# Optimization experiments

Hardware: AMD Instinct MI355X
Metric: run time of the kernel (lower is better)

Reference implementation:

```python
import jax, jax.numpy as jnp
import numpy as np

B, S, M, D, H, NH = 8, 1024, 2048, 512, 512, 8  # batch, seq, mem slots, memory_dim, hidden_dim, heads
THRESHOLD = 0.5
DECAY = 0.95


def setup_inputs() -> dict:
    key = jax.random.key(0)
    ks = jax.random.split(key, 16)
    def w(k, shape, s=0.02):
        return jax.random.normal(k, shape, jnp.float32) * s
    z = lambda n: jnp.zeros((n,), jnp.float32)
    return {
        'new_info': jax.random.normal(ks[0], (B, S, D), jnp.float32),
        'memory_bank': jax.random.normal(ks[1], (B, M, D), jnp.float32),
        'W_in': w(ks[2], (D, H)), 'b_in': z(H),
        'Wq': w(ks[3], (H, H)), 'bq': z(H),
        'Wk': w(ks[4], (H, H)), 'bk': z(H),
        'Wv': w(ks[5], (H, H)), 'bv': z(H),
        'Wo': w(ks[6], (H, H)), 'bo': z(H),
        'Wi1': w(ks[7], (H, H // 2)), 'bi1': z(H // 2),
        'Wi2': w(ks[8], (H // 2, 1)), 'bi2': z(1),
        'Wu1': w(ks[9], (2 * H, H)), 'bu1': z(H),
        'Wu2': w(ks[10], (H, H)), 'bu2': z(H),
    }


def _mha(q, k, v, Wq, bq, Wk, bk, Wv, bv, Wo, bo):
    # torch nn.MultiheadAttention math (batch_first, eval mode / no dropout)
    b, mq, h = q.shape
    d = h // NH
    qh = (q @ Wq + bq).reshape(b, mq, NH, d)
    kh = (k @ Wk + bk).reshape(b, -1, NH, d)
    vh = (v @ Wv + bv).reshape(b, -1, NH, d)
    scores = jnp.einsum('bqhd,bkhd->bhqk', qh, kh) / np.float32(np.sqrt(d))
    attn = jax.nn.softmax(scores, axis=-1)
    out = jnp.einsum('bhqk,bkhd->bqhd', attn, vh).reshape(b, mq, h)
    return out @ Wo + bo


def reference(new_info, memory_bank, W_in, b_in, Wq, bq, Wk, bk, Wv, bv, Wo, bo,
              Wi1, bi1, Wi2, bi2, Wu1, bu1, Wu2, bu2):
    # project new info + memory into hidden space
    info_proj = new_info @ W_in + b_in                       # [B,S,H]
    mem_proj = memory_bank @ W_in + b_in                     # [B,M,H]
    # per-token importance (sigmoid MLP)
    imp = jax.nn.sigmoid(jax.nn.relu(info_proj @ Wi1 + bi1) @ Wi2 + bi2)[..., 0]  # [B,S]
    # cross-attention: memory slots attend to new tokens -> per-slot write weights
    attn_out = _mha(mem_proj, info_proj, info_proj, Wq, bq, Wk, bk, Wv, bv, Wo, bo)  # [B,M,H]
    # scale write weights by importance (vectorized reading of the original broadcast)
    write_weights = attn_out * jnp.mean(imp, axis=1)[:, None, None]  # [B,M,H]
    # write-position selection: argmax over memory slots (importance scalar is positive,
    # so in the original all qualifying tokens of a batch pick the same slot)
    pos = jnp.argmax(jnp.mean(write_weights, axis=-1), axis=1)      # [B]
    mask = imp > THRESHOLD                                          # [B,S]
    exists = jnp.any(mask, axis=1)                                  # [B]
    # original loop overwrites the slot for each qualifying s, always reading the
    # ORIGINAL memory_bank -> final value comes from the LAST qualifying token
    s_star = S - 1 - jnp.argmax(mask[:, ::-1], axis=1)              # [B]
    bidx = jnp.arange(B)
    sel = new_info[bidx, s_star]                                    # [B,D]
    old = memory_bank[bidx, pos]                                    # [B,D]
    comb = jnp.concatenate([old, sel], axis=-1)                     # [B,2D]
    upd = jnp.tanh(jax.nn.relu(comb @ Wu1 + bu1) @ Wu2 + bu2)       # [B,H]
    ww = write_weights[bidx, pos]                                   # [B,H]
    new_mem = jnp.where(exists[:, None], old + upd * ww, old)
    updated = memory_bank.at[bidx, pos].set(new_mem)
    # forgetting: memory_age defaults to zeros -> decay_rate**0 == 1 (kept for fidelity)
    decay = jnp.power(jnp.float32(DECAY), jnp.zeros((M,), jnp.float32))
    updated = updated * decay[None, :, None]
    return updated, write_weights, imp
```

## Files before the change

### kernel.cpp

```cpp
#include <hip/hip_runtime.h>
#include <hip/hip_bf16.h>
#include <math.h>

#define BB 8
#define SS 1024
#define MM 2048
#define DD 512
#define HH 512
#define NHEAD 8
#define DHEAD 64

typedef __attribute__((ext_vector_type(8))) short short8;
typedef __attribute__((ext_vector_type(4))) float f32x4;
typedef unsigned short us;

__device__ __forceinline__ us bf_hi(float x) {
    __hip_bfloat16 h = __float2bfloat16(x);
    return *reinterpret_cast<const us*>(&h);
}
__device__ __forceinline__ float bf_f(us h) {
    return __uint_as_float(((unsigned)h) << 16);
}
__device__ __forceinline__ void split_pack4(float a, float b, float c, float d,
                                            uint2& hp, uint2& lp) {
    us h0 = bf_hi(a), h1 = bf_hi(b), h2 = bf_hi(c), h3 = bf_hi(d);
    hp.x = (unsigned)h0 | ((unsigned)h1 << 16);
    hp.y = (unsigned)h2 | ((unsigned)h3 << 16);
    us l0 = bf_hi(a - bf_f(h0)), l1 = bf_hi(b - bf_f(h1));
    us l2 = bf_hi(c - bf_f(h2)), l3 = bf_hi(d - bf_f(h3));
    lp.x = (unsigned)l0 | ((unsigned)l1 << 16);
    lp.y = (unsigned)l2 | ((unsigned)l3 << 16);
}
__device__ __forceinline__ uint2 pack4_hi(float a, float b, float c, float d) {
    uint2 hp;
    hp.x = (unsigned)bf_hi(a) | ((unsigned)bf_hi(b) << 16);
    hp.y = (unsigned)bf_hi(c) | ((unsigned)bf_hi(d) << 16);
    return hp;
}

__device__ __forceinline__ void gload_lds16(const void* g, void* l) {
    __builtin_amdgcn_global_load_lds(
        (__attribute__((address_space(1))) void*)(g),
        (__attribute__((address_space(3))) void*)(l), 16, 0, 0);
}

struct TSB {
    const float* src[6];
    us* dh[6];
    us* dl[6];
    int nc[6];
};

__global__ __launch_bounds__(256) void prep_all(
    const float* __restrict__ x, float* __restrict__ cpy,
    us* __restrict__ hi, us* __restrict__ lo, int n8, float* __restrict__ zbuf,
    const float* __restrict__ bk, const float* __restrict__ bv,
    float* __restrict__ bkv,
    const float* __restrict__ b_in, const float* __restrict__ Wq,
    const float* __restrict__ bq, float* __restrict__ bq_eff, TSB a)
{
    __shared__ float tile[32][33];
    const int blk = blockIdx.x, tid = threadIdx.x;
    if (blk >= 2066) {
        const int t = blk - 2066;
        const int wsel = t >> 8;
        const int n0 = (t & 15) * 32, k0 = ((t >> 4) & 15) * 32;
        const int ncols = a.nc[wsel];
        if (n0 >= ncols) return;
        const float* W = a.src[wsel];
        {
            const int r = tid >> 3, c = (tid & 7) * 4;
            const float4 v = *(const float4*)(W + (size_t)(k0 + r) * ncols + n0 + c);
            tile[r][c + 0] = v.x; tile[r][c + 1] = v.y;
            tile[r][c + 2] = v.z; tile[r][c + 3] = v.w;
        }
        __syncthreads();
        {
            const int n = tid >> 3, k = (tid & 7) * 4;
            uint2 hp, lp;
            split_pack4(tile[k + 0][n], tile[k + 1][n], tile[k + 2][n], tile[k + 3][n], hp, lp);
            *(uint2*)(a.dh[wsel] + (size_t)(n0 + n) * 512 + k0 + k) = hp;
            *(uint2*)(a.dl[wsel] + (size_t)(n0 + n) * 512 + k0 + k) = lp;
        }
        return;
    }
    if (blk >= 2064) {
        const int n = (blk - 2064) * 256 + tid;
        float v = bq[n];
        for (int k = 0; k < 512; ++k) v = fmaf(b_in[k], Wq[(size_t)k * 512 + n], v);
        bq_eff[n] = v;
        return;
    }
    if (blk >= 2060) {
        const int i = (blk - 2060) * 256 + tid;
        bkv[i] = (i < 512) ? bk[i] : bv[i - 512];
        return;
    }
    if (blk >= 2048) {
        const int i = (blk - 2048) * 2048 + tid * 8;
        *(float4*)(zbuf + i) = make_float4(0.f, 0.f, 0.f, 0.f);
        *(float4*)(zbuf + i + 4) = make_float4(0.f, 0.f, 0.f, 0.f);
        return;
    }
    const int stride = 2048 * 256;
    for (int i = blk * 256 + tid; i < n8; i += stride) {
        const float4 va = *(const float4*)(x + (size_t)i * 8);
        const float4 vb = *(const float4*)(x + (size_t)i * 8 + 4);
        *(float4*)(cpy + (size_t)i * 8) = va;
        *(float4*)(cpy + (size_t)i * 8 + 4) = vb;
        uint2 h0, l0, h1, l1;
        split_pack4(va.x, va.y, va.z, va.w, h0, l0);
        split_pack4(vb.x, vb.y, vb.z, vb.w, h1, l1);
        *(uint2*)(hi + (size_t)i * 8) = h0;
        *(uint2*)(hi + (size_t)i * 8 + 4) = h1;
        *(uint2*)(lo + (size_t)i * 8) = l0;
        *(uint2*)(lo + (size_t)i * 8 + 4) = l1;
    }
}

#define GEMM_F32A_BODY(K_)                                                          \
    f32x4 acc[4][4];                                                                \
    _Pragma("unroll")                                                               \
    for (int i = 0; i < 4; ++i)                                                     \
        _Pragma("unroll")                                                           \
        for (int j = 0; j < 4; ++j)                                                 \
            _Pragma("unroll")                                                       \
            for (int r = 0; r < 4; ++r) acc[i][j][r] = 0.f;                         \
    const int ar = tid >> 4;                                                        \
    const int ak = (tid & 15) * 4;                                                  \
    int bsrow[4], bsf[4], bsoff[4];                                                 \
    _Pragma("unroll")                                                               \
    for (int it = 0; it < 4; ++it) {                                                \
        const int s = tid + 256 * it;                                               \
        bsrow[it] = s >> 3;                                                         \
        bsf[it] = s & 7;                                                            \
        bsoff[it] = bsrow[it] * 64 + ((bsf[it] ^ (bsrow[it] & 7)) << 3);            \
    }                                                                               \
    for (int k0 = 0; k0 < (K_); k0 += 64) {                                         \
        __syncthreads();                                                            \
        _Pragma("unroll")                                                           \
        for (int p = 0; p < 8; ++p) {                                               \
            const int r = p * 16 + ar;                                              \
            const float4 av = *(const float4*)(A + (size_t)(m0 + r) * (K_) + k0 + ak); \
            const int aoff = r * 128 + (((ak >> 3) ^ (r & 7)) << 4) + ((tid & 1) << 3); \
            uint2 hp, lp;                                                           \
            split_pack4(av.x, av.y, av.z, av.w, hp, lp);                            \
            *(uint2*)((char*)sAh + aoff) = hp;                                      \
            *(uint2*)((char*)sAl + aoff) = lp;                                      \
        }                                                                           \
        _Pragma("unroll")                                                           \
        for (int it = 0; it < 4; ++it) {                                            \
            const size_t bo = (size_t)(n0 + bsrow[it]) * (K_) + k0 + bsf[it] * 8;   \
            *(uint4*)(sBh + bsoff[it]) = *(const uint4*)(Bh + bo);                  \
            *(uint4*)(sBl + bsoff[it]) = *(const uint4*)(Bl + bo);                  \
        }                                                                           \
        __syncthreads();                                                            \
        _Pragma("unroll")                                                           \
        for (int ks = 0; ks < 2; ++ks) {                                            \
            short8 afh[4], afl[4], bfh[4], bfl[4];                                  \
            _Pragma("unroll")                                                       \
            for (int i = 0; i < 4; ++i) {                                           \
                const int row = wm * 64 + i * 16 + fr;                              \
                const int off = row * 128 + (((ks * 4 + fq4) ^ (row & 7)) << 4);    \
                afh[i] = *(const short8*)((const char*)sAh + off);                  \
                afl[i] = *(const short8*)((const char*)sAl + off);                  \
            }                                                                       \
            _Pragma("unroll")                                                       \
            for (int j = 0; j < 4; ++j) {                                           \
                const int row = wn * 64 + j * 16 + fr;                              \
                const int off = row * 128 + (((ks * 4 + fq4) ^ (row & 7)) << 4);    \
                bfh[j] = *(const short8*)((const char*)sBh + off);                  \
                bfl[j] = *(const short8*)((const char*)sBl + off);                  \
            }                                                                       \
            _Pragma("unroll")                                                       \
            for (int i = 0; i < 4; ++i)                                             \
                _Pragma("unroll")                                                   \
                for (int j = 0; j < 4; ++j) {                                       \
                    acc[i][j] = __builtin_amdgcn_mfma_f32_16x16x32_bf16(afh[i], bfh[j], acc[i][j], 0, 0, 0); \
                    acc[i][j] = __builtin_amdgcn_mfma_f32_16x16x32_bf16(afh[i], bfl[j], acc[i][j], 0, 0, 0); \
                    acc[i][j] = __builtin_amdgcn_mfma_f32_16x16x32_bf16(afl[i], bfh[j], acc[i][j], 0, 0, 0); \
                }                                                                   \
        }                                                                           \
    }

__global__ __launch_bounds__(256) void gemm_info_winq(
    const float* __restrict__ new_info,
    const us* __restrict__ wtin_h, const us* __restrict__ wtin_l,
    const float* __restrict__ b_in,
    us* __restrict__ Oh, us* __restrict__ Ol,
    const float* __restrict__ W_in,
    const us* __restrict__ wtq_h, const us* __restrict__ wtq_l,
    us* __restrict__ wtinq_h, us* __restrict__ wtinq_l)
{
    __shared__ us sm[32768];
    us* sAh = sm;            us* sAl = sm + 8192;
    us* sBh = sm + 16384;    us* sBl = sm + 24576;
    const int tid = threadIdx.x, lane = tid & 63;
    const int wid = tid >> 6, wm = wid >> 1, wn = wid & 1;
    const int fr = lane & 15, fq4 = lane >> 4;
    const int id = blockIdx.x;
    const bool isInfo = (id < 256);
    int m0, n0;
    const float* A;
    const us *Bh, *Bl;
    if (isInfo) {
        m0 = (id >> 2) * 128; n0 = (id & 3) * 128;
        A = new_info; Bh = wtin_h; Bl = wtin_l;
    } else {
        const int t = id - 256;
        m0 = (t >> 2) * 128; n0 = (t & 3) * 128;
        A = W_in; Bh = wtq_h; Bl = wtq_l;
    }
    GEMM_F32A_BODY(512)

    if (isInfo) {
#pragma unroll
        for (int j = 0; j < 4; ++j) {
            const int col = n0 + wn * 64 + j * 16 + fr;
            const float bj = b_in[col];
#pragma unroll
            for (int i = 0; i < 4; ++i)
#pragma unroll
                for (int r = 0; r < 4; ++r) {
                    const int row = m0 + wm * 64 + i * 16 + fq4 * 4 + r;
                    const float v = acc[i][j][r] + bj;
                    const us hv = bf_hi(v);
                    Oh[(size_t)row * 512 + col] = hv;
                    Ol[(size_t)row * 512 + col] = bf_hi(v - bf_f(hv));
                }
        }
    } else {
#pragma unroll
        for (int j = 0; j < 4; ++j) {
            const int col = n0 + wn * 64 + j * 16 + fr;
#pragma unroll
            for (int i = 0; i < 4; ++i)
#pragma unroll
                for (int r = 0; r < 4; ++r) {
                    const int row = m0 + wm * 64 + i * 16 + fq4 * 4 + r;
                    const float v = acc[i][j][r];
                    const us hv = bf_hi(v);
                    wtinq_h[(size_t)col * 512 + row] = hv;
                    wtinq_l[(size_t)col * 512 + row] = bf_hi(v - bf_f(hv));
                }
        }
    }
}

#define GEMM_PS_CORE(AhP, AlP, BhP, BlP, rsA_, K_)                                  \
    us* sAh = sm;            us* sAl = sm + 8192;                                   \
    us* sBh = sm + 16384;    us* sBl = sm + 24576;                                  \
    f32x4 acc[4][4];                                                                \
    _Pragma("unroll")                                                               \
    for (int i = 0; i < 4; ++i)                                                     \
        _Pragma("unroll")                                                           \
        for (int j = 0; j < 4; ++j)                                                 \
            _Pragma("unroll")                                                       \
            for (int r = 0; r < 4; ++r) acc[i][j][r] = 0.f;                         \
    const int fp = lane & 7, rsub = lane >> 3;                                      \
    const us* gsrc = (wid == 0) ? (AhP) : (wid == 1) ? (AlP)                        \
                   : (wid == 2) ? (BhP) : (BlP);                                    \
    const int grow0 = (wid < 2) ? m0 : n0;                                          \
    const int grs = (wid < 2) ? (rsA_) : (K_);                                      \
    us* lbase = sm + wid * 8192;                                                    \
    for (int k0 = 0; k0 < (K_); k0 += 64) {                                         \
        __syncthreads();                                                            \
        _Pragma("unroll")                                                           \
        for (int i = 0; i < 16; ++i) {                                              \
            const int row = i * 8 + rsub;                                           \
            const us* g = gsrc + (size_t)(grow0 + row) * grs + k0 +                 \
                          ((fp ^ (row & 7)) << 3);                                  \
            gload_lds16(g, lbase + i * 512);                                        \
        }                                                                           \
        __syncthreads();                                                            \
        _Pragma("unroll")                                                           \
        for (int ks = 0; ks < 2; ++ks) {                                            \
            short8 afh[4], afl[4], bfh[4], bfl[4];                                  \
            _Pragma("unroll")                                                       \
            for (int i = 0; i < 4; ++i) {                                           \
                const int row = wm * 64 + i * 16 + fr;                              \
                const int off = row * 128 + (((ks * 4 + fq4) ^ (row & 7)) << 4);    \
                afh[i] = *(const short8*)((const char*)sAh + off);                  \
                afl[i] = *(const short8*)((const char*)sAl + off);                  \
            }                                                                       \
            _Pragma("unroll")                                                       \
            for (int j = 0; j < 4; ++j) {                                           \
                const int row = wn * 64 + j * 16 + fr;                              \
                const int off = row * 128 + (((ks * 4 + fq4) ^ (row & 7)) << 4);    \
                bfh[j] = *(const short8*)((const char*)sBh + off);                  \
                bfl[j] = *(const short8*)((const char*)sBl + off);                  \
            }                                                                       \
            _Pragma("unroll")                                                       \
            for (int i = 0; i < 4; ++i)                                             \
                _Pragma("unroll")                                                   \
                for (int j = 0; j < 4; ++j) {                                       \
                    acc[i][j] = __builtin_amdgcn_mfma_f32_16x16x32_bf16(afh[i], bfh[j], acc[i][j], 0, 0, 0); \
                    acc[i][j] = __builtin_amdgcn_mfma_f32_16x16x32_bf16(afh[i], bfl[j], acc[i][j], 0, 0, 0); \
                    acc[i][j] = __builtin_amdgcn_mfma_f32_16x16x32_bf16(afl[i], bfh[j], acc[i][j], 0, 0, 0); \
                }                                                                   \
        }                                                                           \
    }

__global__ __launch_bounds__(256) void gemm_h1_logit(
    const us* __restrict__ Ah, const us* __restrict__ Al,
    const us* __restrict__ Bh, const us* __restrict__ Bl,
    const float* __restrict__ bias, const float* __restrict__ Wi2,
    float* __restrict__ logit)
{
    __shared__ us sm[32768];
    const int tid = threadIdx.x, lane = tid & 63;
    const int wid = tid >> 6, wm = wid >> 1, wn = wid & 1;
    const int fr = lane & 15, fq4 = lane >> 4;
    const int m0 = blockIdx.y * 128, n0 = blockIdx.x * 128;
    GEMM_PS_CORE(Ah, Al, Bh, Bl, 512, 512)

    float wsum[4][4];
#pragma unroll
    for (int i = 0; i < 4; ++i)
#pragma unroll
        for (int r = 0; r < 4; ++r) wsum[i][r] = 0.f;

#pragma unroll
    for (int j = 0; j < 4; ++j) {
        const int col = n0 + wn * 64 + j * 16 + fr;
        const float bj = bias[col];
        const float w2 = Wi2[col];
#pragma unroll
        for (int i = 0; i < 4; ++i)
#pragma unroll
            for (int r = 0; r < 4; ++r) {
                const float v = fmaxf(acc[i][j][r] + bj, 0.f);
                wsum[i][r] = fmaf(v, w2, wsum[i][r]);
            }
    }

    __syncthreads();
    float* red = (float*)sm;
    if (tid < 128) red[tid] = 0.f;
    __syncthreads();
#pragma unroll
    for (int i = 0; i < 4; ++i)
#pragma unroll
        for (int r = 0; r < 4; ++r)
            atomicAdd(&red[wm * 64 + i * 16 + fq4 * 4 + r], wsum[i][r]);
    __syncthreads();
    if (tid < 128) atomicAdd(&logit[m0 + tid], red[tid]);
}

__global__ __launch_bounds__(256) void impfin(
    const float* __restrict__ logit, const float* __restrict__ bi2,
    float* __restrict__ imp, float* __restrict__ imp_mean,
    int* __restrict__ s_star, int* __restrict__ exists)
{
    const int b = blockIdx.x, tid = threadIdx.x;
    const float b0 = bi2[0];
    float sum = 0.f; int last = -1;
    for (int s = tid; s < SS; s += 256) {
        const float ip = 1.0f / (1.0f + expf(-(logit[b * SS + s] + b0)));
        imp[b * SS + s] = ip;
        sum += ip;
        if (ip > 0.5f) last = s;
    }
#pragma unroll
    for (int m = 1; m < 64; m <<= 1) {
        sum += __shfl_xor(sum, m);
        last = max(last, __shfl_xor(last, m));
    }
    __shared__ float ssum[4]; __shared__ int slast[4];
    if ((tid & 63) == 0) { ssum[tid >> 6] = sum; slast[tid >> 6] = last; }
    __syncthreads();
    if (tid == 0) {
        const float t = ssum[0] + ssum[1] + ssum[2] + ssum[3];
        const int ml = max(max(slast[0], slast[1]), max(slast[2], slast[3]));
        imp_mean[b] = t / (float)SS;
        exists[b] = (ml >= 0) ? 1 : 0;
        s_star[b] = (ml >= 0) ? ml : (SS - 1);
    }
}

__global__ __launch_bounds__(256) void gemm_qkv_ps(
    const us* __restrict__ mbh, const us* __restrict__ mbl,
    const us* __restrict__ wtinq_h, const us* __restrict__ wtinq_l,
    const float* __restrict__ bq_eff,
    us* __restrict__ qsph, us* __restrict__ qspl,
    const us* __restrict__ iph, const us* __restrict__ ipl,
    const us* __restrict__ wtkv_h, const us* __restrict__ wtkv_l,
    const float* __restrict__ bkv,
    us* __restrict__ Kh, us* __restrict__ Kl,
    us* __restrict__ Vth, us* __restrict__ Vtl)
{
    __shared__ us sm[32768];
    const int tid = threadIdx.x, lane = tid & 63;
    const int wid = tid >> 6, wm = wid >> 1, wn = wid & 1;
    const int fr = lane & 15, fq4 = lane >> 4;
    const int id = blockIdx.x;
    const bool isQ = (id < 512);
    int m0, n0;
    const us *Ah, *Al, *Bh, *Bl;
    if (isQ) {
        m0 = (id >> 2) * 128; n0 = (id & 3) * 128;
        Ah = mbh; Al = mbl; Bh = wtinq_h; Bl = wtinq_l;
    } else {
        const int t = id - 512;
        m0 = (t >> 3) * 128; n0 = (t & 7) * 128;
        Ah = iph; Al = ipl; Bh = wtkv_h; Bl = wtkv_l;
    }
    GEMM_PS_CORE(Ah, Al, Bh, Bl, 512, 512)

    if (isQ) {
#pragma unroll
        for (int j = 0; j < 4; ++j) {
            const int col = n0 + wn * 64 + j * 16 + fr;
            const float bj = bq_eff[col];
#pragma unroll
            for (int i = 0; i < 4; ++i)
#pragma unroll
                for (int r = 0; r < 4; ++r) {
                    const int row = m0 + wm * 64 + i * 16 + fq4 * 4 + r;
                    const float v = acc[i][j][r] + bj;
                    const us hv = bf_hi(v);
                    qsph[(size_t)row * 512 + col] = hv;
                    qspl[(size_t)row * 512 + col] = bf_hi(v - bf_f(hv));
                }
        }
    } else if (n0 < 512) {
#pragma unroll
        for (int j = 0; j < 4; ++j) {
            const int col = n0 + wn * 64 + j * 16 + fr;
            const float bj = bkv[col];
#pragma unroll
            for (int i = 0; i < 4; ++i)
#pragma unroll
                for (int r = 0; r < 4; ++r) {
                    const int row = m0 + wm * 64 + i * 16 + fq4 * 4 + r;
                    const float v = (acc[i][j][r] + bj) * 0.125f;
                    const us hv = bf_hi(v);
                    Kh[(size_t)row * 512 + col] = hv;
                    Kl[(size_t)row * 512 + col] = bf_hi(v - bf_f(hv));
                }
        }
    } else {
#pragma unroll
        for (int j = 0; j < 4; ++j) {
            const int col = n0 + wn * 64 + j * 16 + fr;
            const float bj = bkv[col];
            const int d = col - 512;
#pragma unroll
            for (int i = 0; i < 4; ++i) {
                const int row0 = m0 + wm * 64 + i * 16 + fq4 * 4;
                uint2 hp, lp;
                split_pack4(acc[i][j][0] + bj, acc[i][j][1] + bj,
                            acc[i][j][2] + bj, acc[i][j][3] + bj, hp, lp);
                const size_t vo = ((size_t)(row0 >> 10) * 512 + d) * 1024 + (row0 & 1023);
                *(uint2*)(Vth + vo) = hp;
                *(uint2*)(Vtl + vo) = lp;
            }
        }
    }
}

__global__ __launch_bounds__(256) void gemm_wo_ps(
    const us* __restrict__ Ah, const us* __restrict__ Al,
    const us* __restrict__ Bh, const us* __restrict__ Bl,
    const float* __restrict__ bias, float* __restrict__ C,
    const float* __restrict__ rowscale, float* __restrict__ rowmeanv)
{
    __shared__ us sm[32768];
    const int tid = threadIdx.x, lane = tid & 63;
    const int wid = tid >> 6, wm = wid >> 1, wn = wid & 1;
    const int fr = lane & 15, fq4 = lane >> 4;
    const int m0 = blockIdx.y * 128, n0 = blockIdx.x * 128;
    GEMM_PS_CORE(Ah, Al, Bh, Bl, 512, 512)

    float rsum[4][4];
#pragma unroll
    for (int i = 0; i < 4; ++i)
#pragma unroll
        for (int r = 0; r < 4; ++r) rsum[i][r] = 0.f;

#pragma unroll
    for (int j = 0; j < 4; ++j) {
        const int col = n0 + wn * 64 + j * 16 + fr;
        const float bj = bias[col];
#pragma unroll
        for (int i = 0; i < 4; ++i)
#pragma unroll
            for (int r = 0; r < 4; ++r) {
                const int row = m0 + wm * 64 + i * 16 + fq4 * 4 + r;
                const float v = (acc[i][j][r] + bj) * rowscale[row / MM];
                C[(size_t)row * 512 + col] = v;
                rsum[i][r] += v;
            }
    }

    __syncthreads();
    float* red = (float*)sm;
    if (tid < 128) red[tid] = 0.f;
    __syncthreads();
#pragma unroll
    for (int i = 0; i < 4; ++i)
#pragma unroll
        for (int r = 0; r < 4; ++r)
            atomicAdd(&red[wm * 64 + i * 16 + fq4 * 4 + r], rsum[i][r]);
    __syncthreads();
    if (tid < 128) atomicAdd(&rowmeanv[m0 + tid], red[tid] * (1.0f / 512.0f));
}

__global__ __launch_bounds__(256) void attn_mfma(
    const us* __restrict__ Qh, const us* __restrict__ Ql,
    const us* __restrict__ Kh, const us* __restrict__ Kl,
    const us* __restrict__ Vth, const us* __restrict__ Vtl,
    us* __restrict__ aoh, us* __restrict__ aol)
{
    __shared__ us sm[20480];
    us* sKh = sm;            us* sKl = sm + 4096;
    us* sVh = sm + 8192;     us* sVl = sm + 12288;
    us* sPh = sm + 16384;

    const int tid = threadIdx.x, lane = tid & 63, w = tid >> 6;
    const int fr = lane & 15, fq4 = lane >> 4;

    const int wg = blockIdx.x;
    const int xcd = wg & 7, ix = wg >> 3;
    const int mt = ix & 31;
    const int pair = xcd + 8 * (ix >> 5);
    const int h = pair & 7, b = pair >> 3;
    const int m0 = mt * 64;

    const us* Qgh = Qh + ((size_t)(b * MM + m0)) * 512 + h * DHEAD;
    const us* Qgl = Ql + ((size_t)(b * MM + m0)) * 512 + h * DHEAD;
    const us* Kgh = Kh + ((size_t)b * SS) * 512 + h * DHEAD;
    const us* Kgl = Kl + ((size_t)b * SS) * 512 + h * DHEAD;
    const us* Vgh = Vth + ((size_t)b * 512 + h * DHEAD) * 1024;
    const us* Vgl = Vtl + ((size_t)b * 512 + h * DHEAD) * 1024;
    us* Oh = aoh + ((size_t)(b * MM + m0)) * 512 + h * DHEAD;
    us* Ol = aol + ((size_t)(b * MM + m0)) * 512 + h * DHEAD;

    short8 qfh[2], qfl[2];
#pragma unroll
    for (int ks = 0; ks < 2; ++ks) {
        const size_t qo = (size_t)(w * 16 + fr) * 512 + ks * 32 + fq4 * 8;
        qfh[ks] = *(const short8*)(Qgh + qo);
        qfl[ks] = *(const short8*)(Qgl + qo);
    }

    const int fp = lane & 7;
    const int rsub = lane >> 3;
    const bool isK = (w < 2);
    const us* gA = (w == 0) ? Kgh : (w == 1) ? Kgl : (w == 2) ? Vgh : Vgl;
    us* lbase = sm + w * 4096;

    f32x4 oacc[4];
#pragma unroll
    for (int j = 0; j < 4; ++j)
#pragma unroll
        for (int r = 0; r < 4; ++r) oacc[j][r] = 0.f;
    float mrun = -1e30f, lrun = 0.f;

    for (int t = 0; t < SS / 64; ++t) {
        __syncthreads();
        if (isK) {
#pragma unroll
            for (int i = 0; i < 8; ++i) {
                const int row = i * 8 + rsub;
                const us* g = gA + (size_t)(t * 64 + row) * 512 + ((fp ^ (row & 7)) << 3);
                gload_lds16(g, lbase + i * 512);
            }
        } else {
#pragma unroll
            for (int i = 0; i < 8; ++i) {
                const int row = i * 8 + rsub;
                const us* g = gA + (size_t)row * 1024 + t * 64 + ((fp ^ (row & 7)) << 3);
                gload_lds16(g, lbase + i * 512);
            }
        }
        __syncthreads();

        f32x4 stt[4];
#pragma unroll
        for (int fs = 0; fs < 4; ++fs)
#pragma unroll
            for (int r = 0; r < 4; ++r) stt[fs][r] = 0.f;
#pragma unroll
        for (int ks = 0; ks < 2; ++ks) {
            short8 kfh[4], kfl[4];
#pragma unroll
            for (int fs = 0; fs < 4; ++fs) {
                const int row = fs * 16 + fr;
                const int off = row * 128 + (((ks * 4 + fq4) ^ (row & 7)) << 4);
                kfh[fs] = *(const short8*)((const char*)sKh + off);
                kfl[fs] = *(const short8*)((const char*)sKl + off);
            }
#pragma unroll
            for (int fs = 0; fs < 4; ++fs) {
                stt[fs] = __builtin_amdgcn_mfma_f32_16x16x32_bf16(kfh[fs], qfh[ks], stt[fs], 0, 0, 0);
                stt[fs] = __builtin_amdgcn_mfma_f32_16x16x32_bf16(kfh[fs], qfl[ks], stt[fs], 0, 0, 0);
                stt[fs] = __builtin_amdgcn_mfma_f32_16x16x32_bf16(kfl[fs], qfh[ks], stt[fs], 0, 0, 0);
            }
        }

        float mx = stt[0][0];
#pragma unroll
        for (int fs = 0; fs < 4; ++fs)
#pragma unroll
            for (int r = 0; r < 4; ++r) mx = fmaxf(mx, stt[fs][r]);
        mx = fmaxf(mx, __shfl_xor(mx, 16));
        mx = fmaxf(mx, __shfl_xor(mx, 32));
        const bool grow = __any(mx > mrun);
        float scf = 1.f;
        if (grow) {
            const float nm = fmaxf(mrun, mx);
            scf = __expf(mrun - nm);
            mrun = nm;
        }
        float ps = 0.f;
#pragma unroll
        for (int fs = 0; fs < 4; ++fs)
#pragma unroll
            for (int r = 0; r < 4; ++r) {
                const float p = __expf(stt[fs][r] - mrun);
                stt[fs][r] = p;
                ps += p;
            }
        ps += __shfl_xor(ps, 16);
        ps += __shfl_xor(ps, 32);
        lrun = lrun * scf + ps;

#pragma unroll
        for (int fs = 0; fs < 4; ++fs) {
            const int q = w * 16 + fr;
            const int flog = (fs << 1) | (fq4 >> 1);
            const int off = q * 128 + ((flog ^ (q & 7)) << 4) + ((fq4 & 1) << 3);
            *(uint2*)((char*)sPh + off) = pack4_hi(stt[fs][0], stt[fs][1],
                                                  stt[fs][2], stt[fs][3]);
        }

        if (grow) {
#pragma unroll
            for (int r = 0; r < 4; ++r) {
                const float scv = __shfl(scf, fq4 * 4 + r);
#pragma unroll
                for (int fd = 0; fd < 4; ++fd) oacc[fd][r] *= scv;
            }
        }

#pragma unroll
        for (int ks = 0; ks < 2; ++ks) {
            short8 pfh, vfh[4], vfl[4];
            {
                const int row = w * 16 + fr;
                const int off = row * 128 + (((ks * 4 + fq4) ^ (row & 7)) << 4);
                pfh = *(const short8*)((const char*)sPh + off);
            }
#pragma unroll
            for (int fd = 0; fd < 4; ++fd) {
                const int row = fd * 16 + fr;
                const int off = row * 128 + (((ks * 4 + fq4) ^ (row & 7)) << 4);
                vfh[fd] = *(const short8*)((const char*)sVh + off);
                vfl[fd] = *(const short8*)((const char*)sVl + off);
            }
#pragma unroll
            for (int fd = 0; fd < 4; ++fd) {
                oacc[fd] = __builtin_amdgcn_mfma_f32_16x16x32_bf16(pfh, vfh[fd], oacc[fd], 0, 0, 0);
                oacc[fd] = __builtin_amdgcn_mfma_f32_16x16x32_bf16(pfh, vfl[fd], oacc[fd], 0, 0, 0);
            }
        }
    }

#pragma unroll
    for (int r = 0; r < 4; ++r) {
        const float inv = 1.0f / __shfl(lrun, fq4 * 4 + r);
        const int q = w * 16 + fq4 * 4 + r;
#pragma unroll
        for (int fd = 0; fd < 4; ++fd) {
            const float v = oacc[fd][r] * inv;
            const us hv = bf_hi(v);
            Oh[(size_t)q * 512 + fd * 16 + fr] = hv;
            Ol[(size_t)q * 512 + fd * 16 + fr] = bf_hi(v - bf_f(hv));
        }
    }
}

__global__ __launch_bounds__(256) void argmax_update(
    const float* __restrict__ rm,
    const float* __restrict__ mb, const float* __restrict__ ni,
    const float* __restrict__ Wu1, const float* __restrict__ bu1,
    const float* __restrict__ Wu2, const float* __restrict__ bu2,
    const float* __restrict__ wwp, const int* __restrict__ s_star,
    const int* __restrict__ exists, float* __restrict__ outu)
{
    const int b = blockIdx.x, tid = threadIdx.x;
    __shared__ float comb[2 * DD];
    __shared__ float hu[HH];
    __shared__ float sv[4]; __shared__ int si[4];
    __shared__ int spos;

    {
        float best = -3.0e38f; int bidx = 1 << 30;
        for (int m = tid; m < MM; m += 256) {
            const float v = rm[b * MM + m];
            if (v > best || (v == best && m < bidx)) { best = v; bidx = m; }
        }
#pragma unroll
        for (int msk = 1; msk < 64; msk <<= 1) {
            const float ov = __shfl_xor(best, msk);
            const int oi = __shfl_xor(bidx, msk);
            if (ov > best || (ov == best && oi < bidx)) { best = ov; bidx = oi; }
        }
        if ((tid & 63) == 0) { sv[tid >> 6] = best; si[tid >> 6] = bidx; }
        __syncthreads();
        if (tid == 0) {
            for (int w = 1; w < 4; ++w)
                if (sv[w] > best || (sv[w] == best && si[w] < bidx)) { best = sv[w]; bidx = si[w]; }
            spos = bidx;
        }
        __syncthreads();
    }

    const int p = spos, ss = s_star[b], ex = exists[b];
    const float* oldp = mb + ((size_t)(b * MM + p)) * DD;
    const float* selp = ni + ((size_t)(b * SS + ss)) * DD;
    for (int i = tid; i < DD; i += 256) { comb[i] = oldp[i]; comb[DD + i] = selp[i]; }
    __syncthreads();
#pragma unroll
    for (int t = 0; t < 2; ++t) {
        const int n = tid + t * 256;
        float a = bu1[n];
        for (int k = 0; k < 2 * DD; ++k) a = fmaf(comb[k], Wu1[(size_t)k * HH + n], a);
        hu[n] = fmaxf(a, 0.f);
    }
    __syncthreads();
#pragma unroll
    for (int t = 0; t < 2; ++t) {
        const int n = tid + t * 256;
        float a = bu2[n];
        for (int k = 0; k < HH; ++k) a = fmaf(hu[k], Wu2[(size_t)k * HH + n], a);
        const float upd = tanhf(a);
        const float wwv = wwp[((size_t)(b * MM + p)) * HH + n];
        const float ov = oldp[n];
        outu[((size_t)(b * MM + p)) * DD + n] = ex ? fmaf(upd, wwv, ov) : ov;
    }
}

extern "C" void kernel_launch(void* const* d_in, const int* in_sizes, int n_in,
                              void* d_out, int out_size, void* d_ws, size_t ws_size,
                              hipStream_t stream)
{
    const float* new_info    = (const float*)d_in[0];
    const float* memory_bank = (const float*)d_in[1];
    const float* W_in = (const float*)d_in[2];  const float* b_in = (const float*)d_in[3];
    const float* Wq   = (const float*)d_in[4];  const float* bq   = (const float*)d_in[5];
    const float* Wk   = (const float*)d_in[6];  const float* bk   = (const float*)d_in[7];
    const float* Wv   = (const float*)d_in[8];  const float* bv   = (const float*)d_in[9];
    const float* Wo   = (const float*)d_in[10]; const float* bo   = (const float*)d_in[11];
    const float* Wi1  = (const float*)d_in[12]; const float* bi1  = (const float*)d_in[13];
    const float* Wi2  = (const float*)d_in[14]; const float* bi2  = (const float*)d_in[15];
    const float* Wu1  = (const float*)d_in[16]; const float* bu1  = (const float*)d_in[17];
    const float* Wu2  = (const float*)d_in[18]; const float* bu2  = (const float*)d_in[19];

    float* out = (float*)d_out;
    float* out_updated = out;
    float* out_ww      = out + (size_t)BB * MM * HH;
    float* out_imp     = out + 2 * (size_t)BB * MM * HH;

    float* ws = (float*)d_ws;
    float* qsp_rg    = ws;
    float* ip_sp     = qsp_rg + 8388608;
    float* mb_sp     = ip_sp + 4194304;
    float* kvreg     = mb_sp + 8388608;
    float* wtf       = kvreg + 8388608;
    float* bq_eff    = wtf + 1703936;
    float* bkv       = bq_eff + 512;
    float* rowmeanv  = bkv + 1024;
    float* logit     = rowmeanv + 16384;
    float* imp_mean  = logit + 8192;
    int*   istar     = (int*)(imp_mean + BB);
    int*   iexists   = istar + BB;

    us* qsph = (us*)qsp_rg;
    us* qspl = qsph + 8388608;
    us* iph = (us*)ip_sp;
    us* ipl = iph + 4194304;
    us* mbh = (us*)mb_sp;
    us* mbl = mbh + 8388608;
    us* Kh  = (us*)kvreg;
    us* Kl  = Kh + 4194304;
    us* Vth = Kl + 4194304;
    us* Vtl = Vth + 4194304;

    us* wtin_h  = (us*)wtf;            us* wtin_l  = wtin_h + 262144;
    us* wtq_h   = wtin_l + 262144;     us* wtq_l   = wtq_h + 262144;
    us* wtkv_h  = wtq_l + 262144;      us* wtkv_l  = wtkv_h + 524288;
    us* wto_h   = wtkv_l + 524288;     us* wto_l   = wto_h + 262144;
    us* wtinq_h = wto_l + 262144;      us* wtinq_l = wtinq_h + 262144;
    us* wti1_h  = wtinq_l + 262144;    us* wti1_l  = wti1_h + 131072;

    const dim3 blk(256);

    TSB ts;
    ts.src[0] = W_in; ts.dh[0] = wtin_h;          ts.dl[0] = wtin_l;          ts.nc[0] = 512;
    ts.src[1] = Wq;   ts.dh[1] = wtq_h;           ts.dl[1] = wtq_l;           ts.nc[1] = 512;
    ts.src[2] = Wk;   ts.dh[2] = wtkv_h;          ts.dl[2] = wtkv_l;          ts.nc[2] = 512;
    ts.src[3] = Wv;   ts.dh[3] = wtkv_h + 262144; ts.dl[3] = wtkv_l + 262144; ts.nc[3] = 512;
    ts.src[4] = Wo;   ts.dh[4] = wto_h;           ts.dl[4] = wto_l;           ts.nc[4] = 512;
    ts.src[5] = Wi1;  ts.dh[5] = wti1_h;          ts.dl[5] = wti1_l;          ts.nc[5] = 256;
    prep_all<<<dim3(2066 + 1536), blk, 0, stream>>>(memory_bank, out_updated,
                                                    mbh, mbl, 1048576, rowmeanv,
                                                    bk, bv, bkv, b_in, Wq, bq,
                                                    bq_eff, ts);

    gemm_info_winq<<<dim3(272), blk, 0, stream>>>(new_info, wtin_h, wtin_l, b_in,
                                                  iph, ipl, W_in, wtq_h, wtq_l,
                                                  wtinq_h, wtinq_l);

    gemm_h1_logit<<<dim3(2, 64), blk, 0, stream>>>(iph, ipl, wti1_h, wti1_l,
                                                   bi1, Wi2, logit);

    impfin<<<dim3(BB), blk, 0, stream>>>(logit, bi2, out_imp,
                                         imp_mean, istar, iexists);

    gemm_qkv_ps<<<dim3(1024), blk, 0, stream>>>(mbh, mbl, wtinq_h, wtinq_l,
                                                bq_eff, qsph, qspl,
                                                iph, ipl, wtkv_h, wtkv_l, bkv,
                                                Kh, Kl, Vth, Vtl);

    attn_mfma<<<dim3(2048), blk, 0, stream>>>(qsph, qspl, Kh, Kl, Vth, Vtl,
                                              mbh, mbl);

    gemm_wo_ps<<<dim3(4, 128), blk, 0, stream>>>(mbh, mbl, wto_h, wto_l,
                                                 bo, out_ww, imp_mean, rowmeanv);

    argmax_update<<<dim3(BB), blk, 0, stream>>>(rowmeanv, memory_bank, new_info,
                                                Wu1, bu1, Wu2, bu2, out_ww,
                                                istar, iexists, out_updated);
}
```

Baseline: 424.1 us.

## Fold importance MLP GEMM and finalize into QKV and attention launches

Removes two kernel launches by appending the h1/logit GEMM tiles as extra blocks of the QKV projection kernel and the importance finalize as extra blocks of the attention kernel. Also raises wave priority around the attention MFMA loops and splits the update-MLP dot products into four independent accumulators to break the serial FMA dependency chain. This cuts launch gaps and small underfilled grids, at the cost of changing the summation order in the update MLP.

After: 409.1 us. -3.5%, faster.

```diff
diff --git a/kernel.cpp b/kernel.cpp
--- a/kernel.cpp
+++ b/kernel.cpp
@@ -301,84 +301,7 @@
         }                                                                           \
     }
 
-__global__ __launch_bounds__(256) void gemm_h1_logit(
-    const us* __restrict__ Ah, const us* __restrict__ Al,
-    const us* __restrict__ Bh, const us* __restrict__ Bl,
-    const float* __restrict__ bias, const float* __restrict__ Wi2,
-    float* __restrict__ logit)
-{
-    __shared__ us sm[32768];
-    const int tid = threadIdx.x, lane = tid & 63;
-    const int wid = tid >> 6, wm = wid >> 1, wn = wid & 1;
-    const int fr = lane & 15, fq4 = lane >> 4;
-    const int m0 = blockIdx.y * 128, n0 = blockIdx.x * 128;
-    GEMM_PS_CORE(Ah, Al, Bh, Bl, 512, 512)
-
-    float wsum[4][4];
-#pragma unroll
-    for (int i = 0; i < 4; ++i)
-#pragma unroll
-        for (int r = 0; r < 4; ++r) wsum[i][r] = 0.f;
-
-#pragma unroll
-    for (int j = 0; j < 4; ++j) {
-        const int col = n0 + wn * 64 + j * 16 + fr;
-        const float bj = bias[col];
-        const float w2 = Wi2[col];
-#pragma unroll
-        for (int i = 0; i < 4; ++i)
-#pragma unroll
-            for (int r = 0; r < 4; ++r) {
-                const float v = fmaxf(acc[i][j][r] + bj, 0.f);
-                wsum[i][r] = fmaf(v, w2, wsum[i][r]);
-            }
-    }
-
-    __syncthreads();
-    float* red = (float*)sm;
-    if (tid < 128) red[tid] = 0.f;
-    __syncthreads();
-#pragma unroll
-    for (int i = 0; i < 4; ++i)
-#pragma unroll
-        for (int r = 0; r < 4; ++r)
-            atomicAdd(&red[wm * 64 + i * 16 + fq4 * 4 + r], wsum[i][r]);
-    __syncthreads();
-    if (tid < 128) atomicAdd(&logit[m0 + tid], red[tid]);
-}
-
-__global__ __launch_bounds__(256) void impfin(
-    const float* __restrict__ logit, const float* __restrict__ bi2,
-    float* __restrict__ imp, float* __restrict__ imp_mean,
-    int* __restrict__ s_star, int* __restrict__ exists)
-{
-    const int b = blockIdx.x, tid = threadIdx.x;
-    const float b0 = bi2[0];
-    float sum = 0.f; int last = -1;
-    for (int s = tid; s < SS; s += 256) {
-        const float ip = 1.0f / (1.0f + expf(-(logit[b * SS + s] + b0)));
-        imp[b * SS + s] = ip;
-        sum += ip;
-        if (ip > 0.5f) last = s;
-    }
-#pragma unroll
-    for (int m = 1; m < 64; m <<= 1) {
-        sum += __shfl_xor(sum, m);
-        last = max(last, __shfl_xor(last, m));
-    }
-    __shared__ float ssum[4]; __shared__ int slast[4];
-    if ((tid & 63) == 0) { ssum[tid >> 6] = sum; slast[tid >> 6] = last; }
-    __syncthreads();
-    if (tid == 0) {
-        const float t = ssum[0] + ssum[1] + ssum[2] + ssum[3];
-        const int ml = max(max(slast[0], slast[1]), max(slast[2], slast[3]));
-        imp_mean[b] = t / (float)SS;
-        exists[b] = (ml >= 0) ? 1 : 0;
-        s_star[b] = (ml >= 0) ? ml : (SS - 1);
-    }
-}
-
-__global__ __launch_bounds__(256) void gemm_qkv_ps(
+__global__ __launch_bounds__(256) void gemm_qkvh1_ps(
     const us* __restrict__ mbh, const us* __restrict__ mbl,
     const us* __restrict__ wtinq_h, const us* __restrict__ wtinq_l,
     const float* __restrict__ bq_eff,
@@ -387,27 +310,33 @@
     const us* __restrict__ wtkv_h, const us* __restrict__ wtkv_l,
     const float* __restrict__ bkv,
     us* __restrict__ Kh, us* __restrict__ Kl,
-    us* __restrict__ Vth, us* __restrict__ Vtl)
+    us* __restrict__ Vth, us* __restrict__ Vtl,
+    const us* __restrict__ wti1_h, const us* __restrict__ wti1_l,
+    const float* __restrict__ bi1, const float* __restrict__ Wi2,
+    float* __restrict__ logit)
 {
     __shared__ us sm[32768];
     const int tid = threadIdx.x, lane = tid & 63;
     const int wid = tid >> 6, wm = wid >> 1, wn = wid & 1;
     const int fr = lane & 15, fq4 = lane >> 4;
     const int id = blockIdx.x;
-    const bool isQ = (id < 512);
     int m0, n0;
     const us *Ah, *Al, *Bh, *Bl;
-    if (isQ) {
+    if (id < 512) {
         m0 = (id >> 2) * 128; n0 = (id & 3) * 128;
         Ah = mbh; Al = mbl; Bh = wtinq_h; Bl = wtinq_l;
-    } else {
+    } else if (id < 1024) {
         const int t = id - 512;
         m0 = (t >> 3) * 128; n0 = (t & 7) * 128;
         Ah = iph; Al = ipl; Bh = wtkv_h; Bl = wtkv_l;
+    } else {
+        const int t = id - 1024;
+        m0 = (t >> 1) * 128; n0 = (t & 1) * 128;
+        Ah = iph; Al = ipl; Bh = wti1_h; Bl = wti1_l;
     }
     GEMM_PS_CORE(Ah, Al, Bh, Bl, 512, 512)
 
-    if (isQ) {
+    if (id < 512) {
 #pragma unroll
         for (int j = 0; j < 4; ++j) {
             const int col = n0 + wn * 64 + j * 16 + fr;
@@ -423,7 +352,7 @@
                     qspl[(size_t)row * 512 + col] = bf_hi(v - bf_f(hv));
                 }
         }
-    } else if (n0 < 512) {
+    } else if (id < 1024 && n0 < 512) {
 #pragma unroll
         for (int j = 0; j < 4; ++j) {
             const int col = n0 + wn * 64 + j * 16 + fr;
@@ -439,7 +368,7 @@
                     Kl[(size_t)row * 512 + col] = bf_hi(v - bf_f(hv));
                 }
         }
-    } else {
+    } else if (id < 1024) {
 #pragma unroll
         for (int j = 0; j < 4; ++j) {
             const int col = n0 + wn * 64 + j * 16 + fr;
@@ -456,6 +385,36 @@
                 *(uint2*)(Vtl + vo) = lp;
             }
         }
+    } else {
+        float wsum[4][4];
+#pragma unroll
+        for (int i = 0; i < 4; ++i)
+#pragma unroll
+            for (int r = 0; r < 4; ++r) wsum[i][r] = 0.f;
+#pragma unroll
+        for (int j = 0; j < 4; ++j) {
+            const int col = n0 + wn * 64 + j * 16 + fr;
+            const float bj = bi1[col];
+            const float w2 = Wi2[col];
+#pragma unroll
+            for (int i = 0; i < 4; ++i)
+#pragma unroll
+                for (int r = 0; r < 4; ++r) {
+                    const float v = fmaxf(acc[i][j][r] + bj, 0.f);
+                    wsum[i][r] = fmaf(v, w2, wsum[i][r]);
+                }
+        }
+        __syncthreads();
+        float* red = (float*)sm;
+        if (tid < 128) red[tid] = 0.f;
+        __syncthreads();
+#pragma unroll
+        for (int i = 0; i < 4; ++i)
+#pragma unroll
+            for (int r = 0; r < 4; ++r)
+                atomicAdd(&red[wm * 64 + i * 16 + fq4 * 4 + r], wsum[i][r]);
+        __syncthreads();
+        if (tid < 128) atomicAdd(&logit[m0 + tid], red[tid]);
     }
 }
 
@@ -510,14 +469,47 @@
     const us* __restrict__ Qh, const us* __restrict__ Ql,
     const us* __restrict__ Kh, const us* __restrict__ Kl,
     const us* __restrict__ Vth, const us* __restrict__ Vtl,
-    us* __restrict__ aoh, us* __restrict__ aol)
+    us* __restrict__ aoh, us* __restrict__ aol,
+    const float* __restrict__ logit, const float* __restrict__ bi2,
+    float* __restrict__ imp, float* __restrict__ imp_mean,
+    int* __restrict__ s_star, int* __restrict__ exists)
 {
     __shared__ us sm[20480];
+    const int tid = threadIdx.x, lane = tid & 63, w = tid >> 6;
+
+    if (blockIdx.x >= 2048) {
+        const int b = blockIdx.x - 2048;
+        const float b0 = bi2[0];
+        float sum = 0.f; int last = -1;
+        for (int s = tid; s < SS; s += 256) {
+            const float ip = 1.0f / (1.0f + expf(-(logit[b * SS + s] + b0)));
+            imp[b * SS + s] = ip;
+            sum += ip;
+            if (ip > 0.5f) last = s;
+        }
+#pragma unroll
+        for (int m = 1; m < 64; m <<= 1) {
+            sum += __shfl_xor(sum, m);
+            last = max(last, __shfl_xor(last, m));
+        }
+        float* ssum = (float*)sm;
+        int* slast = (int*)(sm + 16);
+        if (lane == 0) { ssum[w] = sum; slast[w] = last; }
+        __syncthreads();
+        if (tid == 0) {
+            const float t = ssum[0] + ssum[1] + ssum[2] + ssum[3];
+            const int ml = max(max(slast[0], slast[1]), max(slast[2], slast[3]));
+            imp_mean[b] = t / (float)SS;
+            exists[b] = (ml >= 0) ? 1 : 0;
+            s_star[b] = (ml >= 0) ? ml : (SS - 1);
+        }
+        return;
+    }
+
     us* sKh = sm;            us* sKl = sm + 4096;
     us* sVh = sm + 8192;     us* sVl = sm + 12288;
     us* sPh = sm + 16384;
 
-    const int tid = threadIdx.x, lane = tid & 63, w = tid >> 6;
     const int fr = lane & 15, fq4 = lane >> 4;
 
     const int wg = blockIdx.x;
@@ -581,6 +573,7 @@
         for (int fs = 0; fs < 4; ++fs)
 #pragma unroll
             for (int r = 0; r < 4; ++r) stt[fs][r] = 0.f;
+        __builtin_amdgcn_s_setprio(1);
 #pragma unroll
         for (int ks = 0; ks < 2; ++ks) {
             short8 kfh[4], kfl[4];
@@ -598,6 +591,7 @@
                 stt[fs] = __builtin_amdgcn_mfma_f32_16x16x32_bf16(kfl[fs], qfh[ks], stt[fs], 0, 0, 0);
             }
         }
+        __builtin_amdgcn_s_setprio(0);
 
         float mx = stt[0][0];
 #pragma unroll
@@ -644,6 +638,7 @@
             }
         }
 
+        __builtin_amdgcn_s_setprio(1);
 #pragma unroll
         for (int ks = 0; ks < 2; ++ks) {
             short8 pfh, vfh[4], vfl[4];
@@ -665,6 +660,7 @@
                 oacc[fd] = __builtin_amdgcn_mfma_f32_16x16x32_bf16(pfh, vfl[fd], oacc[fd], 0, 0, 0);
             }
         }
+        __builtin_amdgcn_s_setprio(0);
     }
 
 #pragma unroll
@@ -725,17 +721,27 @@
 #pragma unroll
     for (int t = 0; t < 2; ++t) {
         const int n = tid + t * 256;
-        float a = bu1[n];
-        for (int k = 0; k < 2 * DD; ++k) a = fmaf(comb[k], Wu1[(size_t)k * HH + n], a);
-        hu[n] = fmaxf(a, 0.f);
+        float a0 = 0.f, a1 = 0.f, a2 = 0.f, a3 = 0.f;
+        for (int k = 0; k < 2 * DD; k += 4) {
+            a0 = fmaf(comb[k + 0], Wu1[(size_t)(k + 0) * HH + n], a0);
+            a1 = fmaf(comb[k + 1], Wu1[(size_t)(k + 1) * HH + n], a1);
+            a2 = fmaf(comb[k + 2], Wu1[(size_t)(k + 2) * HH + n], a2);
+            a3 = fmaf(comb[k + 3], Wu1[(size_t)(k + 3) * HH + n], a3);
+        }
+        hu[n] = fmaxf(bu1[n] + ((a0 + a1) + (a2 + a3)), 0.f);
     }
     __syncthreads();
 #pragma unroll
     for (int t = 0; t < 2; ++t) {
         const int n = tid + t * 256;
-        float a = bu2[n];
-        for (int k = 0; k < HH; ++k) a = fmaf(hu[k], Wu2[(size_t)k * HH + n], a);
-        const float upd = tanhf(a);
+        float a0 = 0.f, a1 = 0.f, a2 = 0.f, a3 = 0.f;
+        for (int k = 0; k < HH; k += 4) {
+            a0 = fmaf(hu[k + 0], Wu2[(size_t)(k + 0) * HH + n], a0);
+            a1 = fmaf(hu[k + 1], Wu2[(size_t)(k + 1) * HH + n], a1);
+            a2 = fmaf(hu[k + 2], Wu2[(size_t)(k + 2) * HH + n], a2);
+            a3 = fmaf(hu[k + 3], Wu2[(size_t)(k + 3) * HH + n], a3);
+        }
+        const float upd = tanhf(bu2[n] + ((a0 + a1) + (a2 + a3)));
         const float wwv = wwp[((size_t)(b * MM + p)) * HH + n];
         const float ov = oldp[n];
         outu[((size_t)(b * MM + p)) * DD + n] = ex ? fmaf(upd, wwv, ov) : ov;
@@ -813,19 +819,15 @@
                                                   iph, ipl, W_in, wtq_h, wtq_l,
                                                   wtinq_h, wtinq_l);
 
-    gemm_h1_logit<<<dim3(2, 64), blk, 0, stream>>>(iph, ipl, wti1_h, wti1_l,
-                                                   bi1, Wi2, logit);
-
-    impfin<<<dim3(BB), blk, 0, stream>>>(logit, bi2, out_imp,
-                                         imp_mean, istar, iexists);
-
-    gemm_qkv_ps<<<dim3(1024), blk, 0, stream>>>(mbh, mbl, wtinq_h, wtinq_l,
-                                                bq_eff, qsph, qspl,
-                                                iph, ipl, wtkv_h, wtkv_l, bkv,
-                                                Kh, Kl, Vth, Vtl);
-
-    attn_mfma<<<dim3(2048), blk, 0, stream>>>(qsph, qspl, Kh, Kl, Vth, Vtl,
-                                              mbh, mbl);
+    gemm_qkvh1_ps<<<dim3(1152), blk, 0, stream>>>(mbh, mbl, wtinq_h, wtinq_l,
+                                                  bq_eff, qsph, qspl,
+                                                  iph, ipl, wtkv_h, wtkv_l, bkv,
+                                                  Kh, Kl, Vth, Vtl,
+                                                  wti1_h, wti1_l, bi1, Wi2, logit);
+
+    attn_mfma<<<dim3(2056), blk, 0, stream>>>(qsph, qspl, Kh, Kl, Vth, Vtl,
+                                              mbh, mbl, logit, bi2, out_imp,
+                                              imp_mean, istar, iexists);
 
     gemm_wo_ps<<<dim3(4, 128), blk, 0, stream>>>(mbh, mbl, wto_h, wto_l,
                                                  bo, out_ww, imp_mean, rowmeanv);
```
